# Optimization experiments

Measured on AMD Instinct MI355X. Metric: run time of the kernel, lower is better.

## Reference

```python
import jax, jax.numpy as jnp
import numpy as np

D = 1024
HEADS = 16
HEAD_DIM = D // HEADS
EPS = 1e-5


def layer_norm(x, gamma, beta):
    mu = jnp.mean(x, axis=-1, keepdims=True)
    var = jnp.mean(jnp.square(x - mu), axis=-1, keepdims=True)
    return (x - mu) * jax.lax.rsqrt(var + EPS) * gamma + beta


def setup_inputs() -> dict:
    key = jax.random.key(0)
    ks = jax.random.split(key, 8)
    B, S = 4, 2048
    s_in = 1.0 / np.sqrt(D)
    s_ffn = 1.0 / np.sqrt(4 * D)
    return {
        "x": jax.random.normal(ks[0], (B, S, D), dtype=jnp.float32),
        "ln1_g": jnp.ones((D,), jnp.float32),
        "ln1_b": jnp.zeros((D,), jnp.float32),
        "w_qkv": jax.random.uniform(ks[1], (D, 3 * D), jnp.float32, -s_in, s_in),
        "b_qkv": jnp.zeros((3 * D,), jnp.float32),
        "w_out": jax.random.uniform(ks[2], (D, D), jnp.float32, -s_in, s_in),
        "b_out": jnp.zeros((D,), jnp.float32),
        "ln2_g": jnp.ones((D,), jnp.float32),
        "ln2_b": jnp.zeros((D,), jnp.float32),
        "w_ffn1": jax.random.uniform(ks[3], (D, 4 * D), jnp.float32, -s_in, s_in),
        "b_ffn1": jnp.zeros((4 * D,), jnp.float32),
        "w_ffn2": jax.random.uniform(ks[4], (4 * D, D), jnp.float32, -s_ffn, s_ffn),
        "b_ffn2": jnp.zeros((D,), jnp.float32),
    }


def reference(x, ln1_g, ln1_b, w_qkv, b_qkv, w_out, b_out,
              ln2_g, ln2_b, w_ffn1, b_ffn1, w_ffn2, b_ffn2):
    B, S, Dm = x.shape
    h = layer_norm(x, ln1_g, ln1_b)
    qkv = h @ w_qkv + b_qkv  # [B,S,3D]
    q, k, v = jnp.split(qkv, 3, axis=-1)
    # [B,S,D] -> [B,H,S,hd]
    def to_heads(t):
        return t.reshape(B, S, HEADS, HEAD_DIM).transpose(0, 2, 1, 3)
    q, k, v = to_heads(q), to_heads(k), to_heads(v)
    scores = jnp.einsum('bhqd,bhkd->bhqk', q, k) / np.sqrt(HEAD_DIM).astype(np.float32)
    attn = jax.nn.softmax(scores, axis=-1)
    out = jnp.einsum('bhqk,bhkd->bhqd', attn, v)
    out = out.transpose(0, 2, 1, 3).reshape(B, S, Dm)
    x = x + (out @ w_out + b_out)
    h = layer_norm(x, ln2_g, ln2_b)
    h = jax.nn.gelu(h @ w_ffn1 + b_ffn1, approximate=False) @ w_ffn2 + b_ffn2
    return x + h
```

## Files before the change

kernel.cpp:

```cpp
#include <hip/hip_runtime.h>
#include <cstdint>
#include <cstddef>

typedef unsigned short u16;
typedef unsigned int   u32;
typedef __bf16 bf16x8 __attribute__((ext_vector_type(8)));
typedef float  f32x4  __attribute__((ext_vector_type(4)));
static_assert(sizeof(bf16x8) == 16, "bf16x8 must be 16B");
static_assert(sizeof(f32x4) == 16, "f32x4 must be 16B");

#define DEVI static __device__ __forceinline__

DEVI u16 f2bf(float x) {
  u32 u = __builtin_bit_cast(u32, x);
  u = (u + 0x7FFFu + ((u >> 16) & 1u)) >> 16;
  return (u16)u;
}

DEVI void gload16(const u16* g, u16* l) {
  __builtin_amdgcn_global_load_lds(
      (const __attribute__((address_space(1))) void*)g,
      (__attribute__((address_space(3))) void*)l, 16, 0, 0);
}

#define S_BARRIER() asm volatile("s_barrier" ::: "memory")
#define VMCNT(n) asm volatile("s_waitcnt vmcnt(" #n ")" ::: "memory")

template <int MO, int NACC>
DEVI void mm16(f32x4 (&acc)[NACC][4], const bf16x8 (&af)[4], const bf16x8 (&bf)[4]) {
  __builtin_amdgcn_s_setprio(1);
#pragma unroll
  for (int m = 0; m < 4; m++)
#pragma unroll
    for (int n = 0; n < 4; n++)
      acc[MO + m][n] =
          __builtin_amdgcn_mfma_f32_16x16x32_bf16(af[m], bf[n], acc[MO + m][n], 0, 0, 0);
  __builtin_amdgcn_s_setprio(0);
}

__global__ __launch_bounds__(256) void transpose_cvt(const float* __restrict__ W,
                                                     u16* __restrict__ WT,
                                                     int K, int N) {
  __shared__ float tile[32][33];
  int tx = threadIdx.x & 31, ty = threadIdx.x >> 5;
  int c0 = blockIdx.x * 32, r0 = blockIdx.y * 32;
#pragma unroll
  for (int i = 0; i < 4; i++)
    tile[ty + i * 8][tx] = W[(size_t)(r0 + ty + i * 8) * N + c0 + tx];
  __syncthreads();
#pragma unroll
  for (int i = 0; i < 4; i++) {
    int r = ty + i * 8;
    WT[(size_t)(c0 + r) * K + r0 + tx] = f2bf(tile[tx][r]);
  }
}

__global__ __launch_bounds__(256) void ln_k(const float* __restrict__ X,
                                            const float* __restrict__ gam,
                                            const float* __restrict__ bet,
                                            u16* __restrict__ H) {
  __shared__ float2 part[4];
  int row = blockIdx.x, t = threadIdx.x;
  const float4* xr = (const float4*)(X + (size_t)row * 1024);
  float4 v = xr[t];
  float s = v.x + v.y + v.z + v.w;
  float q = v.x * v.x + v.y * v.y + v.z * v.z + v.w * v.w;
#pragma unroll
  for (int o = 32; o > 0; o >>= 1) {
    s += __shfl_xor(s, o);
    q += __shfl_xor(q, o);
  }
  if ((t & 63) == 0) part[t >> 6] = make_float2(s, q);
  __syncthreads();
  float S = part[0].x + part[1].x + part[2].x + part[3].x;
  float Q = part[0].y + part[1].y + part[2].y + part[3].y;
  float mu = S * (1.f / 1024.f);
  float rs = rsqrtf(Q * (1.f / 1024.f) - mu * mu + 1e-5f);
  float4 gv = ((const float4*)gam)[t];
  float4 bv = ((const float4*)bet)[t];
  ushort4 o;
  o.x = f2bf((v.x - mu) * rs * gv.x + bv.x);
  o.y = f2bf((v.y - mu) * rs * gv.y + bv.y);
  o.z = f2bf((v.z - mu) * rs * gv.z + bv.z);
  o.w = f2bf((v.w - mu) * rs * gv.w + bv.w);
  *(ushort4*)(H + (size_t)row * 1024 + t * 4) = o;
}

template <int EPI, int NACC>
DEVI void epilogue(f32x4 (&acc)[NACC][4], const float* bias, const float* res,
                   float* outF, u16* outB, int N, int rbase, int cbase, int g, int li) {
#pragma unroll
  for (int n = 0; n < 4; n++) {
    int c = cbase + n * 16 + li;
    float bv = bias[c];
#pragma unroll
    for (int a = 0; a < NACC; a++) {
      int rowb = rbase + a * 16 + g * 4;
#pragma unroll
      for (int r = 0; r < 4; r++) {
        size_t idx = (size_t)(rowb + r) * N + c;
        float v = acc[a][n][r] + bv;
        if constexpr (EPI == 1) {
          v += res[idx];
          outF[idx] = v;
        } else if constexpr (EPI == 2) {
          v = 0.5f * v * (1.f + erff(v * 0.70710678118654752f));
          outB[idx] = f2bf(v);
        } else {
          outB[idx] = f2bf(v);
        }
      }
    }
  }
}

template <int EPI>
__global__ __launch_bounds__(512, 1) void gemm256(const u16* __restrict__ A,
                                                  const u16* __restrict__ Bt,
                                                  const float* __restrict__ bias,
                                                  const float* __restrict__ res,
                                                  float* __restrict__ outF,
                                                  u16* __restrict__ outB,
                                                  int M, int N, int K) {
  __shared__ uint4 As[2][2048];
  __shared__ uint4 Bs[2][2048];
  const int t = threadIdx.x, lane = t & 63, wv = t >> 6;
  const int wr = wv >> 2, wc = wv & 3;
  const int li = lane & 15, g = lane >> 4;

  const int gx = gridDim.x;
  const int nwg = gx * gridDim.y;
  const int wg = blockIdx.y * gx + blockIdx.x;
  const int swz = (wg & 7) * (nwg >> 3) + (wg >> 3);
  const int bx = swz % gx, by = swz / gx;
  const int bm0 = by * 256, bn0 = bx * 256;

  f32x4 acc[8][4];
  const f32x4 z4 = {0.f, 0.f, 0.f, 0.f};
#pragma unroll
  for (int a = 0; a < 8; a++)
#pragma unroll
    for (int n = 0; n < 4; n++) acc[a][n] = z4;

  const u16* aB = A + (size_t)(bm0 + wv * 16 + li) * K + g * 8;
  const u16* bB = Bt + (size_t)(bn0 + wv * 16 + li) * K + g * 8;
  const size_t rskip = (size_t)128 * K;

  auto stA = [&](int buf, int j, int kt) {
    gload16(aB + (size_t)kt * 64 + ((j & 1) ? rskip : (size_t)0) + (j >> 1) * 32,
            (u16*)&As[buf][(j * 8 + wv) * 64]);
  };
  auto stB = [&](int buf, int j, int kt) {
    gload16(bB + (size_t)kt * 64 + ((j & 1) ? rskip : (size_t)0) + (j >> 1) * 32,
            (u16*)&Bs[buf][(j * 8 + wv) * 64]);
  };

  stA(0, 0, 0); stA(0, 1, 0); stB(0, 0, 0); stB(0, 1, 0);
  stA(0, 2, 0); stA(0, 3, 0); stB(0, 2, 0); stB(0, 3, 0);
  VMCNT(4);
  S_BARRIER();

  const int NT = K >> 6;
  int cur = 0;
  for (int kt = 0; kt < NT; kt++) {
    const int nx = cur ^ 1;
    const bool more = (kt + 1 < NT);
    bf16x8 af[4], bf[4];
#pragma unroll
    for (int n = 0; n < 4; n++)
      bf[n] = __builtin_bit_cast(bf16x8, Bs[cur][(wc * 4 + n) * 64 + lane]);
#pragma unroll
    for (int m = 0; m < 4; m++)
      af[m] = __builtin_bit_cast(bf16x8, As[cur][(wr * 8 + m) * 64 + lane]);
    if (more) { stA(nx, 0, kt + 1); stA(nx, 1, kt + 1); }
    S_BARRIER();
    mm16<0>(acc, af, bf);
    S_BARRIER();
#pragma unroll
    for (int m = 0; m < 4; m++)
      af[m] = __builtin_bit_cast(bf16x8, As[cur][(wr * 8 + 4 + m) * 64 + lane]);
    if (more) { stB(nx, 0, kt + 1); stB(nx, 1, kt + 1); }
    S_BARRIER();
    mm16<4>(acc, af, bf);
    if (more) { VMCNT(4); } else { VMCNT(0); }
    S_BARRIER();
#pragma unroll
    for (int n = 0; n < 4; n++)
      bf[n] = __builtin_bit_cast(bf16x8, Bs[cur][(16 + wc * 4 + n) * 64 + lane]);
#pragma unroll
    for (int m = 0; m < 4; m++)
      af[m] = __builtin_bit_cast(bf16x8, As[cur][(16 + wr * 8 + m) * 64 + lane]);
    if (more) { stA(nx, 2, kt + 1); stA(nx, 3, kt + 1); }
    S_BARRIER();
    mm16<0>(acc, af, bf);
    S_BARRIER();
#pragma unroll
    for (int m = 0; m < 4; m++)
      af[m] = __builtin_bit_cast(bf16x8, As[cur][(16 + wr * 8 + 4 + m) * 64 + lane]);
    if (more) { stB(nx, 2, kt + 1); stB(nx, 3, kt + 1); }
    S_BARRIER();
    mm16<4>(acc, af, bf);
    if (more) { VMCNT(4); }
    S_BARRIER();
    cur = nx;
  }

  epilogue<EPI>(acc, bias, res, outF, outB, N, bm0 + wr * 128, bn0 + wc * 64, g, li);
}

template <int EPI>
__global__ __launch_bounds__(512, 1) void gemm128(const u16* __restrict__ A,
                                                  const u16* __restrict__ Bt,
                                                  const float* __restrict__ bias,
                                                  const float* __restrict__ res,
                                                  float* __restrict__ outF,
                                                  u16* __restrict__ outB,
                                                  int M, int N, int K) {
  __shared__ uint4 As[2][1024];
  __shared__ uint4 Bs[2][2048];
  const int t = threadIdx.x, lane = t & 63, wv = t >> 6;
  const int wr = wv >> 2, wc = wv & 3;
  const int li = lane & 15, g = lane >> 4;

  const int gx = gridDim.x;
  const int nwg = gx * gridDim.y;
  const int wg = blockIdx.y * gx + blockIdx.x;
  const int swz = (wg & 7) * (nwg >> 3) + (wg >> 3);
  const int bx = swz % gx, by = swz / gx;
  const int bm0 = by * 128, bn0 = bx * 256;

  f32x4 acc[4][4];
  const f32x4 z4 = {0.f, 0.f, 0.f, 0.f};
#pragma unroll
  for (int a = 0; a < 4; a++)
#pragma unroll
    for (int n = 0; n < 4; n++) acc[a][n] = z4;

  const u16* aB = A + (size_t)(bm0 + wv * 16 + li) * K + g * 8;
  const u16* bB = Bt + (size_t)(bn0 + wv * 16 + li) * K + g * 8;
  const size_t rskip = (size_t)128 * K;

  auto stA = [&](int buf, int j, int kt) {
    gload16(aB + (size_t)kt * 64 + j * 32, (u16*)&As[buf][(j * 8 + wv) * 64]);
  };
  auto stB = [&](int buf, int j, int kt) {
    gload16(bB + (size_t)kt * 64 + ((j & 1) ? rskip : (size_t)0) + (j >> 1) * 32,
            (u16*)&Bs[buf][(j * 8 + wv) * 64]);
  };

  stA(0, 0, 0); stB(0, 0, 0); stB(0, 1, 0);
  stA(0, 1, 0); stB(0, 2, 0); stB(0, 3, 0);
  VMCNT(3);
  S_BARRIER();

  const int NT = K >> 6;
  int cur = 0;
  for (int kt = 0; kt < NT; kt++) {
    const int nx = cur ^ 1;
    const bool more = (kt + 1 < NT);
    bf16x8 af[4], bf[4];
#pragma unroll
    for (int n = 0; n < 4; n++)
      bf[n] = __builtin_bit_cast(bf16x8, Bs[cur][(wc * 4 + n) * 64 + lane]);
#pragma unroll
    for (int m = 0; m < 4; m++)
      af[m] = __builtin_bit_cast(bf16x8, As[cur][(wr * 4 + m) * 64 + lane]);
    if (more) { stA(nx, 0, kt + 1); stB(nx, 0, kt + 1); stB(nx, 1, kt + 1); }
    S_BARRIER();
    mm16<0>(acc, af, bf);
    if (more) { VMCNT(3); } else { VMCNT(0); }
    S_BARRIER();
#pragma unroll
    for (int n = 0; n < 4; n++)
      bf[n] = __builtin_bit_cast(bf16x8, Bs[cur][(16 + wc * 4 + n) * 64 + lane]);
#pragma unroll
    for (int m = 0; m < 4; m++)
      af[m] = __builtin_bit_cast(bf16x8, As[cur][(8 + wr * 4 + m) * 64 + lane]);
    if (more) { stA(nx, 1, kt + 1); stB(nx, 2, kt + 1); stB(nx, 3, kt + 1); }
    S_BARRIER();
    mm16<0>(acc, af, bf);
    if (more) { VMCNT(3); }
    S_BARRIER();
    cur = nx;
  }

  epilogue<EPI>(acc, bias, res, outF, outB, N, bm0 + wr * 64, bn0 + wc * 64, g, li);
}

__global__ __launch_bounds__(256) void v_tr(const u16* __restrict__ qkv,
                                            u16* __restrict__ vfm) {
  __shared__ u16 Vl[64 * 72];
  const int t = threadIdx.x;
  const int bh = blockIdx.y;
  const int bb = bh >> 4, h = bh & 15;
  const int kt = blockIdx.x;
#pragma unroll
  for (int bq = 0; bq < 2; bq++) {
    int c = t + bq * 256;
    int key = c >> 3, d0 = (c & 7) * 8;
    uint4 v = *(const uint4*)(qkv + (size_t)(bb * 2048 + kt * 64 + key) * 3072 + 2048 +
                              h * 64 + d0);
    *(uint4*)&Vl[key * 72 + d0] = v;
  }
  __syncthreads();
#pragma unroll
  for (int bq = 0; bq < 2; bq++) {
    int oc = t + bq * 256;
    int f = oc >> 6, l = oc & 63;
    int db = f >> 1, g32 = f & 1;
    int li = l & 15, g = l >> 4;
    u16 tmp[8];
#pragma unroll
    for (int e = 0; e < 8; e++) {
      int pk = g32 * 32 + ((e & 4) << 2) + g * 4 + (e & 3);
      tmp[e] = Vl[pk * 72 + db * 16 + li];
    }
    *(uint4*)(vfm + ((((size_t)bh * 32 + kt) * 8 + f) * 64 + l) * 8) = *(uint4*)tmp;
  }
}

__global__ __launch_bounds__(256) void attn_k(const u16* __restrict__ qkv,
                                              const u16* __restrict__ vfm,
                                              u16* __restrict__ ao) {
  __shared__ uint4 Ks[512];
  __shared__ uint4 Vs[512];
  const int t = threadIdx.x, lane = t & 63, wv = t >> 6;
  const int g = lane >> 4, li = lane & 15;
  const int bb = blockIdx.y >> 4, h = blockIdx.y & 15;
  const int q0 = blockIdx.x * 64 + wv * 16;

  const size_t qoff = (size_t)(bb * 2048 + q0 + li) * 3072 + h * 64 + g * 8;
  bf16x8 qf0 = __builtin_bit_cast(bf16x8, *(const uint4*)(qkv + qoff));
  bf16x8 qf1 = __builtin_bit_cast(bf16x8, *(const uint4*)(qkv + qoff + 32));

  const u16* kbase = qkv + (size_t)bb * 2048 * 3072 + 1024 + h * 64;
  const int f1 = wv + 4;
  const u16* ksrc0 = kbase + (size_t)(((wv >> 1) << 4) + li) * 3072 + ((wv & 1) << 5) + g * 8;
  const u16* ksrc1 = kbase + (size_t)(((f1 >> 1) << 4) + li) * 3072 + ((f1 & 1) << 5) + g * 8;
  const u16* vsrc0 = vfm + ((size_t)(bb * 16 + h) * 32) * 4096 + (wv * 64 + lane) * 8;
  const u16* vsrc1 = vsrc0 + 4 * 64 * 8;

  const f32x4 z4 = {0.f, 0.f, 0.f, 0.f};
  f32x4 Of[4];
#pragma unroll
  for (int db = 0; db < 4; db++) Of[db] = z4;
  float m_run = -INFINITY, l_run = 0.f;

  for (int tile = 0; tile < 32; tile++) {
    __syncthreads();
    gload16(ksrc0 + (size_t)tile * 64 * 3072, (u16*)&Ks[wv * 64]);
    gload16(ksrc1 + (size_t)tile * 64 * 3072, (u16*)&Ks[(wv + 4) * 64]);
    gload16(vsrc0 + (size_t)tile * 4096, (u16*)&Vs[wv * 64]);
    gload16(vsrc1 + (size_t)tile * 4096, (u16*)&Vs[(wv + 4) * 64]);
    __syncthreads();

    float sc[16];
    float mt = -INFINITY;
#pragma unroll
    for (int g32 = 0; g32 < 2; g32++) {
#pragma unroll
      for (int tt = 0; tt < 2; tt++) {
        int kb16 = g32 * 2 + tt;
        bf16x8 k0f = __builtin_bit_cast(bf16x8, Ks[(kb16 * 2 + 0) * 64 + lane]);
        bf16x8 k1f = __builtin_bit_cast(bf16x8, Ks[(kb16 * 2 + 1) * 64 + lane]);
        f32x4 st = z4;
        st = __builtin_amdgcn_mfma_f32_16x16x32_bf16(k0f, qf0, st, 0, 0, 0);
        st = __builtin_amdgcn_mfma_f32_16x16x32_bf16(k1f, qf1, st, 0, 0, 0);
#pragma unroll
        for (int r = 0; r < 4; r++) {
          float s = st[r] * 0.125f;
          sc[g32 * 8 + tt * 4 + r] = s;
          mt = fmaxf(mt, s);
        }
      }
    }
    mt = fmaxf(mt, __shfl_xor(mt, 16));
    mt = fmaxf(mt, __shfl_xor(mt, 32));
    float mn = fmaxf(m_run, mt);
    float aa = __expf(m_run - mn);
    float ps = 0.f;
#pragma unroll
    for (int i = 0; i < 16; i++) {
      float p = __expf(sc[i] - mn);
      sc[i] = p;
      ps += p;
    }
    ps += __shfl_xor(ps, 16);
    ps += __shfl_xor(ps, 32);
    l_run = l_run * aa + ps;
    m_run = mn;
    float a0 = __shfl(aa, g * 4 + 0);
    float a1 = __shfl(aa, g * 4 + 1);
    float a2 = __shfl(aa, g * 4 + 2);
    float a3 = __shfl(aa, g * 4 + 3);
#pragma unroll
    for (int db = 0; db < 4; db++) {
      Of[db][0] *= a0;
      Of[db][1] *= a1;
      Of[db][2] *= a2;
      Of[db][3] *= a3;
    }
#pragma unroll
    for (int g32 = 0; g32 < 2; g32++) {
      bf16x8 pf;
#pragma unroll
      for (int j = 0; j < 8; j++) pf[j] = (__bf16)sc[g32 * 8 + j];
#pragma unroll
      for (int db = 0; db < 4; db++) {
        bf16x8 vf = __builtin_bit_cast(bf16x8, Vs[(db * 2 + g32) * 64 + lane]);
        Of[db] = __builtin_amdgcn_mfma_f32_16x16x32_bf16(pf, vf, Of[db], 0, 0, 0);
      }
    }
  }

  float invl[4];
#pragma unroll
  for (int r = 0; r < 4; r++) invl[r] = 1.f / __shfl(l_run, g * 4 + r);
#pragma unroll
  for (int db = 0; db < 4; db++)
#pragma unroll
    for (int r = 0; r < 4; r++)
      ao[(size_t)(bb * 2048 + q0 + 4 * g + r) * 1024 + h * 64 + db * 16 + li] =
          f2bf(Of[db][r] * invl[r]);
}

extern "C" void kernel_launch(void* const* d_in, const int* in_sizes, int n_in,
                              void* d_out, int out_size, void* d_ws, size_t ws_size,
                              hipStream_t stream) {
  const float* x = (const float*)d_in[0];
  const float* ln1g = (const float*)d_in[1];
  const float* ln1b = (const float*)d_in[2];
  const float* wqkv = (const float*)d_in[3];
  const float* bqkv = (const float*)d_in[4];
  const float* wout = (const float*)d_in[5];
  const float* bout = (const float*)d_in[6];
  const float* ln2g = (const float*)d_in[7];
  const float* ln2b = (const float*)d_in[8];
  const float* wff1 = (const float*)d_in[9];
  const float* bff1 = (const float*)d_in[10];
  const float* wff2 = (const float*)d_in[11];
  const float* bff2 = (const float*)d_in[12];
  float* outF = (float*)d_out;
  char* ws = (char*)d_ws;

  u16* wqkvT = (u16*)(ws + 0);
  u16* woutT = (u16*)(ws + 6291456);
  u16* wff1T = (u16*)(ws + 8388608);
  u16* wff2T = (u16*)(ws + 16777216);
  u16* hbuf  = (u16*)(ws + 25165824);
  u16* vfm   = (u16*)(ws + 25165824);
  u16* qkvb  = (u16*)(ws + 41943040);
  u16* attnb = (u16*)(ws + 92274688);
  u16* ffn1b = qkvb;

  transpose_cvt<<<dim3(96, 32), 256, 0, stream>>>(wqkv, wqkvT, 1024, 3072);
  transpose_cvt<<<dim3(32, 32), 256, 0, stream>>>(wout, woutT, 1024, 1024);
  transpose_cvt<<<dim3(128, 32), 256, 0, stream>>>(wff1, wff1T, 1024, 4096);
  transpose_cvt<<<dim3(32, 128), 256, 0, stream>>>(wff2, wff2T, 4096, 1024);

  ln_k<<<8192, 256, 0, stream>>>(x, ln1g, ln1b, hbuf);
  gemm256<0><<<dim3(12, 32), 512, 0, stream>>>(hbuf, wqkvT, bqkv, nullptr, nullptr, qkvb,
                                               8192, 3072, 1024);
  v_tr<<<dim3(32, 64), 256, 0, stream>>>(qkvb, vfm);
  attn_k<<<dim3(32, 64), 256, 0, stream>>>(qkvb, vfm, attnb);
  gemm128<1><<<dim3(4, 64), 512, 0, stream>>>(attnb, woutT, bout, x, outF, nullptr,
                                              8192, 1024, 1024);
  ln_k<<<8192, 256, 0, stream>>>(outF, ln2g, ln2b, hbuf);
  gemm256<2><<<dim3(16, 32), 512, 0, stream>>>(hbuf, wff1T, bff1, nullptr, nullptr, ffn1b,
                                               8192, 4096, 1024);
  gemm128<1><<<dim3(4, 64), 512, 0, stream>>>(ffn1b, wff2T, bff2, outF, outF, nullptr,
                                              8192, 1024, 4096);

  (void)in_sizes;
  (void)n_in;
  (void)out_size;
  (void)ws_size;
}
```

Baseline: 492.9 us.

## Fold softmax scale into Q weights, widen attention KV tile, lazily rescale

Folds 1/sqrt(d)*log2(e) into the Q columns of the QKV weight and bias during preprocessing, so the attention kernel can use exp2 directly with no per-score multiply. Doubles the attention K/V tile from 64 to 128 keys per iteration, halving the loop trips and the barriers per key. Skips the online-softmax rescale of the output and running sum unless the running max grows by more than 8 (in log2 units). The trade-offs are twice the LDS per block, more registers for the scores, and a wider range of unnormalized values before the lazy rescale. The scaled bias is placed in the attention-output buffer, which the attention kernel overwrites later.

```diff
diff --git a/kernel.cpp b/kernel.cpp
--- a/kernel.cpp
+++ b/kernel.cpp
@@ -11,6 +11,8 @@
 
 #define DEVI static __device__ __forceinline__
 
+#define QSCALE 0.18033688011112042f
+
 DEVI u16 f2bf(float x) {
   u32 u = __builtin_bit_cast(u32, x);
   u = (u + 0x7FFFu + ((u >> 16) & 1u)) >> 16;
@@ -40,7 +42,8 @@
 
 __global__ __launch_bounds__(256) void transpose_cvt(const float* __restrict__ W,
                                                      u16* __restrict__ WT,
-                                                     int K, int N) {
+                                                     int K, int N,
+                                                     float scale, int nscale) {
   __shared__ float tile[32][33];
   int tx = threadIdx.x & 31, ty = threadIdx.x >> 5;
   int c0 = blockIdx.x * 32, r0 = blockIdx.y * 32;
@@ -51,8 +54,16 @@
 #pragma unroll
   for (int i = 0; i < 4; i++) {
     int r = ty + i * 8;
-    WT[(size_t)(c0 + r) * K + r0 + tx] = f2bf(tile[tx][r]);
-  }
+    int n = c0 + r;
+    float scl = (n < nscale) ? scale : 1.f;
+    WT[(size_t)n * K + r0 + tx] = f2bf(tile[tx][r] * scl);
+  }
+}
+
+__global__ __launch_bounds__(256) void prep_bias(const float* __restrict__ b,
+                                                 float* __restrict__ o) {
+  int i = blockIdx.x * 256 + threadIdx.x;
+  o[i] = b[i] * (i < 1024 ? QSCALE : 1.f);
 }
 
 __global__ __launch_bounds__(256) void ln_k(const float* __restrict__ X,
@@ -322,8 +333,8 @@
 __global__ __launch_bounds__(256) void attn_k(const u16* __restrict__ qkv,
                                               const u16* __restrict__ vfm,
                                               u16* __restrict__ ao) {
-  __shared__ uint4 Ks[512];
-  __shared__ uint4 Vs[512];
+  __shared__ uint4 Ks[1024];
+  __shared__ uint4 Vs[1024];
   const int t = threadIdx.x, lane = t & 63, wv = t >> 6;
   const int g = lane >> 4, li = lane & 15;
   const int bb = blockIdx.y >> 4, h = blockIdx.y & 15;
@@ -334,11 +345,15 @@
   bf16x8 qf1 = __builtin_bit_cast(bf16x8, *(const uint4*)(qkv + qoff + 32));
 
   const u16* kbase = qkv + (size_t)bb * 2048 * 3072 + 1024 + h * 64;
-  const int f1 = wv + 4;
-  const u16* ksrc0 = kbase + (size_t)(((wv >> 1) << 4) + li) * 3072 + ((wv & 1) << 5) + g * 8;
-  const u16* ksrc1 = kbase + (size_t)(((f1 >> 1) << 4) + li) * 3072 + ((f1 & 1) << 5) + g * 8;
-  const u16* vsrc0 = vfm + ((size_t)(bb * 16 + h) * 32) * 4096 + (wv * 64 + lane) * 8;
-  const u16* vsrc1 = vsrc0 + 4 * 64 * 8;
+  const u16* ksrc[4];
+  const u16* vsrc[4];
+  const u16* vbase = vfm + (size_t)(bb * 16 + h) * 32 * 4096;
+#pragma unroll
+  for (int j = 0; j < 4; j++) {
+    int f = wv + j * 4;
+    ksrc[j] = kbase + (size_t)(((f >> 1) << 4) + li) * 3072 + ((f & 1) << 5) + g * 8;
+    vsrc[j] = vbase + (size_t)(f >> 3) * 4096 + ((f & 7) * 64 + lane) * 8;
+  }
 
   const f32x4 z4 = {0.f, 0.f, 0.f, 0.f};
   f32x4 Of[4];
@@ -346,68 +361,74 @@
   for (int db = 0; db < 4; db++) Of[db] = z4;
   float m_run = -INFINITY, l_run = 0.f;
 
-  for (int tile = 0; tile < 32; tile++) {
+  for (int tile = 0; tile < 16; tile++) {
     __syncthreads();
-    gload16(ksrc0 + (size_t)tile * 64 * 3072, (u16*)&Ks[wv * 64]);
-    gload16(ksrc1 + (size_t)tile * 64 * 3072, (u16*)&Ks[(wv + 4) * 64]);
-    gload16(vsrc0 + (size_t)tile * 4096, (u16*)&Vs[wv * 64]);
-    gload16(vsrc1 + (size_t)tile * 4096, (u16*)&Vs[(wv + 4) * 64]);
+#pragma unroll
+    for (int j = 0; j < 4; j++) {
+      int f = wv + j * 4;
+      gload16(ksrc[j] + (size_t)tile * 128 * 3072, (u16*)&Ks[f * 64]);
+      gload16(vsrc[j] + (size_t)tile * 8192, (u16*)&Vs[f * 64]);
+    }
     __syncthreads();
 
-    float sc[16];
+    float sc[32];
     float mt = -INFINITY;
 #pragma unroll
-    for (int g32 = 0; g32 < 2; g32++) {
-#pragma unroll
-      for (int tt = 0; tt < 2; tt++) {
-        int kb16 = g32 * 2 + tt;
-        bf16x8 k0f = __builtin_bit_cast(bf16x8, Ks[(kb16 * 2 + 0) * 64 + lane]);
-        bf16x8 k1f = __builtin_bit_cast(bf16x8, Ks[(kb16 * 2 + 1) * 64 + lane]);
-        f32x4 st = z4;
-        st = __builtin_amdgcn_mfma_f32_16x16x32_bf16(k0f, qf0, st, 0, 0, 0);
-        st = __builtin_amdgcn_mfma_f32_16x16x32_bf16(k1f, qf1, st, 0, 0, 0);
-#pragma unroll
-        for (int r = 0; r < 4; r++) {
-          float s = st[r] * 0.125f;
-          sc[g32 * 8 + tt * 4 + r] = s;
-          mt = fmaxf(mt, s);
-        }
+    for (int kb = 0; kb < 8; kb++) {
+      bf16x8 k0f = __builtin_bit_cast(bf16x8, Ks[(kb * 2 + 0) * 64 + lane]);
+      bf16x8 k1f = __builtin_bit_cast(bf16x8, Ks[(kb * 2 + 1) * 64 + lane]);
+      f32x4 st = z4;
+      st = __builtin_amdgcn_mfma_f32_16x16x32_bf16(k0f, qf0, st, 0, 0, 0);
+      st = __builtin_amdgcn_mfma_f32_16x16x32_bf16(k1f, qf1, st, 0, 0, 0);
+      const int g32 = kb >> 1, tt = kb & 1;
+#pragma unroll
+      for (int r = 0; r < 4; r++) {
+        float s = st[r];
+        sc[g32 * 8 + tt * 4 + r] = s;
+        mt = fmaxf(mt, s);
       }
     }
     mt = fmaxf(mt, __shfl_xor(mt, 16));
     mt = fmaxf(mt, __shfl_xor(mt, 32));
-    float mn = fmaxf(m_run, mt);
-    float aa = __expf(m_run - mn);
+
+    if (!__all(mt - m_run <= 8.f)) {
+      float mn = fmaxf(m_run, mt);
+      float aa = exp2f(m_run - mn);
+      l_run *= aa;
+      float a0 = __shfl(aa, g * 4 + 0);
+      float a1 = __shfl(aa, g * 4 + 1);
+      float a2 = __shfl(aa, g * 4 + 2);
+      float a3 = __shfl(aa, g * 4 + 3);
+#pragma unroll
+      for (int db = 0; db < 4; db++) {
+        Of[db][0] *= a0;
+        Of[db][1] *= a1;
+        Of[db][2] *= a2;
+        Of[db][3] *= a3;
+      }
+      m_run = mn;
+    }
+
     float ps = 0.f;
 #pragma unroll
-    for (int i = 0; i < 16; i++) {
-      float p = __expf(sc[i] - mn);
+    for (int i = 0; i < 32; i++) {
+      float p = exp2f(sc[i] - m_run);
       sc[i] = p;
       ps += p;
     }
     ps += __shfl_xor(ps, 16);
     ps += __shfl_xor(ps, 32);
-    l_run = l_run * aa + ps;
-    m_run = mn;
-    float a0 = __shfl(aa, g * 4 + 0);
-    float a1 = __shfl(aa, g * 4 + 1);
-    float a2 = __shfl(aa, g * 4 + 2);
-    float a3 = __shfl(aa, g * 4 + 3);
-#pragma unroll
-    for (int db = 0; db < 4; db++) {
-      Of[db][0] *= a0;
-      Of[db][1] *= a1;
-      Of[db][2] *= a2;
-      Of[db][3] *= a3;
-    }
-#pragma unroll
-    for (int g32 = 0; g32 < 2; g32++) {
+    l_run += ps;
+
+#pragma unroll
+    for (int g32 = 0; g32 < 4; g32++) {
       bf16x8 pf;
 #pragma unroll
       for (int j = 0; j < 8; j++) pf[j] = (__bf16)sc[g32 * 8 + j];
+      const int fb = (g32 >> 1) * 8 + (g32 & 1);
 #pragma unroll
       for (int db = 0; db < 4; db++) {
-        bf16x8 vf = __builtin_bit_cast(bf16x8, Vs[(db * 2 + g32) * 64 + lane]);
+        bf16x8 vf = __builtin_bit_cast(bf16x8, Vs[(fb + db * 2) * 64 + lane]);
         Of[db] = __builtin_amdgcn_mfma_f32_16x16x32_bf16(pf, vf, Of[db], 0, 0, 0);
       }
     }
@@ -452,14 +473,16 @@
   u16* qkvb  = (u16*)(ws + 41943040);
   u16* attnb = (u16*)(ws + 92274688);
   u16* ffn1b = qkvb;
-
-  transpose_cvt<<<dim3(96, 32), 256, 0, stream>>>(wqkv, wqkvT, 1024, 3072);
-  transpose_cvt<<<dim3(32, 32), 256, 0, stream>>>(wout, woutT, 1024, 1024);
-  transpose_cvt<<<dim3(128, 32), 256, 0, stream>>>(wff1, wff1T, 1024, 4096);
-  transpose_cvt<<<dim3(32, 128), 256, 0, stream>>>(wff2, wff2T, 4096, 1024);
+  float* biasq = (float*)attnb;
+
+  transpose_cvt<<<dim3(96, 32), 256, 0, stream>>>(wqkv, wqkvT, 1024, 3072, QSCALE, 1024);
+  transpose_cvt<<<dim3(32, 32), 256, 0, stream>>>(wout, woutT, 1024, 1024, 1.f, 0);
+  transpose_cvt<<<dim3(128, 32), 256, 0, stream>>>(wff1, wff1T, 1024, 4096, 1.f, 0);
+  transpose_cvt<<<dim3(32, 128), 256, 0, stream>>>(wff2, wff2T, 4096, 1024, 1.f, 0);
+  prep_bias<<<12, 256, 0, stream>>>(bqkv, biasq);
 
   ln_k<<<8192, 256, 0, stream>>>(x, ln1g, ln1b, hbuf);
-  gemm256<0><<<dim3(12, 32), 512, 0, stream>>>(hbuf, wqkvT, bqkv, nullptr, nullptr, qkvb,
+  gemm256<0><<<dim3(12, 32), 512, 0, stream>>>(hbuf, wqkvT, biasq, nullptr, nullptr, qkvb,
                                                8192, 3072, 1024);
   v_tr<<<dim3(32, 64), 256, 0, stream>>>(qkvb, vfm);
   attn_k<<<dim3(32, 64), 256, 0, stream>>>(qkvb, vfm, attnb);
```

After: 497.1 us. No clear change (+0.9%).
